# Performance work log

Hardware: AMD Instinct MI355X
Metric: run time of the kernel (lower is better)

## Reference

```python
import jax, jax.numpy as jnp
import numpy as np

N_NODES = 100000
N_EDGES = 1600000
D_IN, D_HID, D_OUT = 256, 256, 128


def setup_inputs() -> dict:
    key = jax.random.key(0)
    k1, k2, k3, k4, k5, k6 = jax.random.split(key, 6)
    x = jax.random.normal(k1, (N_NODES, D_IN), dtype=jnp.float32)
    edge_index = jax.random.randint(k2, (2, N_EDGES), 0, N_NODES, dtype=jnp.int64)
    W1 = jax.random.normal(k3, (D_IN, D_HID), dtype=jnp.float32) / np.sqrt(D_IN)
    b1 = jax.random.normal(k4, (D_HID,), dtype=jnp.float32) * 0.01
    W2 = jax.random.normal(k5, (D_HID, D_OUT), dtype=jnp.float32) / np.sqrt(D_HID)
    b2 = jax.random.normal(k6, (D_OUT,), dtype=jnp.float32) * 0.01
    return {"x": x, "edge_index": edge_index, "W1": W1, "b1": b1, "W2": W2, "b2": b2}


def _gcn_conv(x, src, dst, W, b, n_nodes):
    # PyG GCNConv: linear transform, add self-loops, symmetric normalization,
    # scatter-add aggregation, bias.
    h = x @ W                                         # [N, D_out]
    # degree including self-loop (edge weight 1)
    deg = jax.ops.segment_sum(jnp.ones((src.shape[0],), h.dtype), dst,
                              num_segments=n_nodes) + 1.0
    dinv = jax.lax.rsqrt(deg)                         # [N]
    norm = dinv[src] * dinv[dst]                      # [E]
    msg = h[src] * norm[:, None]                      # [E, D_out] gather + scale
    agg = jax.ops.segment_sum(msg, dst, num_segments=n_nodes)
    # self-loop contribution: norm_ii = dinv_i^2
    agg = agg + h * (dinv * dinv)[:, None]
    return agg + b


def reference(x, edge_index, W1, b1, W2, b2):
    src, dst = edge_index[0], edge_index[1]
    n = x.shape[0]
    h = _gcn_conv(x, src, dst, W1, b1, n)
    h = jax.nn.relu(h)
    out = _gcn_conv(h, src, dst, W2, b2, n)
    return out
```

## Files before the change

kernel.cpp:

```cpp
#include <hip/hip_runtime.h>

#define N_NODES 100000
#define N_EDGES 1600000
#define D_IN 256
#define D_HID 256
#define D_OUT 128
#define SLOTS 64

#define NB 1024
#define NPB 98
#define CAP 2048
#define BIN_T 8192
#define BIN_BLKS ((N_EDGES + BIN_T - 1) / BIN_T)
#define GEMM1_ROWTILES ((N_NODES + 127) / 128)
#define GEMM1_BLKS (GEMM1_ROWTILES * 2)

typedef unsigned int u32;
typedef unsigned short u16;
typedef __attribute__((ext_vector_type(8))) short bf16x8;
typedef __attribute__((ext_vector_type(8))) unsigned short u16x8;
typedef __attribute__((ext_vector_type(4))) float f32x4;

__device__ __forceinline__ u16 f2bf(float v) {
    u32 u = __float_as_uint(v);
    u32 r = (u + 0x7fffu + ((u >> 16) & 1u)) >> 16;
    return (u16)r;
}
__device__ __forceinline__ float bf2f(u16 b) {
    return __uint_as_float(((u32)b) << 16);
}

__global__ __launch_bounds__(256) void weights_kernel(
    const float* __restrict__ W1, u16* __restrict__ w1hi,
    const float* __restrict__ W2, u16* __restrict__ w2hi,
    int* __restrict__ gcnt) {
    const int gtid = blockIdx.x * 256 + threadIdx.x;
    const int gstride = gridDim.x * 256;
    for (int i = gtid; i < NB; i += gstride) gcnt[i] = 0;
    for (int i = gtid; i < D_IN * D_HID; i += gstride) {
        const int k = i / D_HID, n = i - k * D_HID;
        w1hi[(size_t)n * D_IN + k] = f2bf(W1[i]);
    }
    for (int i = gtid; i < D_HID * D_OUT; i += gstride) {
        const int k = i / D_OUT, n = i - k * D_OUT;
        w2hi[(size_t)n * D_HID + k] = f2bf(W2[i]);
    }
}

__global__ __launch_bounds__(256) void fused_bin_gemm1(
    const int* __restrict__ src, const int* __restrict__ dst,
    int* __restrict__ gcnt, int* __restrict__ binned,
    const float* __restrict__ x, const u16* __restrict__ B,
    u16* __restrict__ Cb) {
    __shared__ char smem[49152];
    const int t = threadIdx.x;

    if (blockIdx.x < BIN_BLKS) {
        int* hist = (int*)smem;
        int* cur = hist + NB;
        const int base = blockIdx.x * BIN_T;
#pragma unroll
        for (int q = 0; q < NB / 256; ++q) hist[q * 256 + t] = 0;
        __syncthreads();
#pragma unroll 4
        for (int j = 0; j < BIN_T / 256; ++j) {
            const int e = base + j * 256 + t;
            if (e < N_EDGES) atomicAdd(&hist[dst[e] / NPB], 1);
        }
        __syncthreads();
#pragma unroll
        for (int q = 0; q < NB / 256; ++q) {
            const int b = q * 256 + t;
            const int c = hist[b];
            cur[b] = c ? atomicAdd(&gcnt[b], c) : 0;
        }
        __syncthreads();
#pragma unroll 4
        for (int j = 0; j < BIN_T / 256; ++j) {
            const int e = base + j * 256 + t;
            if (e < N_EDGES) {
                const int d = dst[e];
                const int b = d / NPB;
                const int ld = d - b * NPB;
                const int r = atomicAdd(&cur[b], 1);
                if (r < CAP) binned[(size_t)b * CAP + r] = (ld << 17) | src[e];
            }
        }
        return;
    }

    const int bid = blockIdx.x - BIN_BLKS;
    const int mBase = (bid >> 1) * 128;
    const int nBase = (bid & 1) * 128;
    constexpr int ABYTES = 16384;
    constexpr int BUF = ABYTES + 8192;
    const int wave = t >> 6;
    const int lane = t & 63;
    const int wm = wave >> 1, wn = wave & 1;
    const int K = D_IN, N = D_HID, M = N_NODES;

    f32x4 acc[4][4];
#pragma unroll
    for (int i = 0; i < 4; ++i)
#pragma unroll
        for (int j = 0; j < 4; ++j) acc[i][j] = (f32x4){0.f, 0.f, 0.f, 0.f};

    const int lr = lane >> 3;
    const int lp = lane & 7;
    const int lc = lp ^ lr;
    const int lr4 = lane >> 2;
    const int lc4 = (lane & 3) ^ (lr4 & 3);

    auto STAGE = [&](int buf, int kt) {
        const int k0 = kt * 32;
        char* ldsbuf = smem + buf * BUF;
        {
            const int coff = k0 + lc * 4;
#pragma unroll
            for (int q = 0; q < 4; ++q) {
                const int row = wave * 32 + q * 8 + lr;
                int mg = mBase + row;
                if (mg > M - 1) mg = M - 1;
                const float* s = x + (size_t)mg * K + coff;
                char* d = ldsbuf + (wave * 32 + q * 8) * 128;
                __builtin_amdgcn_global_load_lds(
                    (const __attribute__((address_space(1))) u32*)s,
                    (__attribute__((address_space(3))) u32*)d, 16, 0, 0);
            }
        }
        {
            const int coff = k0 + lc4 * 8;
#pragma unroll
            for (int q = 0; q < 2; ++q) {
                const int row = wave * 32 + q * 16 + lr4;
                const int ng = nBase + row;
                const u16* s = B + (size_t)ng * K + coff;
                char* d = ldsbuf + ABYTES + (wave * 32 + q * 16) * 64;
                __builtin_amdgcn_global_load_lds(
                    (const __attribute__((address_space(1))) u32*)s,
                    (__attribute__((address_space(3))) u32*)d, 16, 0, 0);
            }
        }
    };

    auto COMPUTE = [&](int buf) {
        const char* pa = smem + buf * BUF;
        const char* pb = pa + ABYTES;
        const int lm = lane & 15;
        const int c4 = lane >> 4;
        bf16x8 ah[4], bh[4];
#pragma unroll
        for (int i = 0; i < 4; ++i) {
            const int r = wm * 64 + i * 16 + lm;
            const int s = r & 7;
            const f32x4 a0 = *(const f32x4*)(pa + r * 128 + ((2 * c4) ^ s) * 16);
            const f32x4 a1 = *(const f32x4*)(pa + r * 128 + ((2 * c4 + 1) ^ s) * 16);
            bf16x8 h;
#pragma unroll
            for (int j = 0; j < 4; ++j)
                h[j] = (short)((__float_as_uint(a0[j]) + 0x8000u) >> 16);
#pragma unroll
            for (int j = 0; j < 4; ++j)
                h[4 + j] = (short)((__float_as_uint(a1[j]) + 0x8000u) >> 16);
            ah[i] = h;
        }
#pragma unroll
        for (int j = 0; j < 4; ++j) {
            const int r = wn * 64 + j * 16 + lm;
            bh[j] = *(const bf16x8*)(pb + r * 64 + (c4 ^ (r & 3)) * 16);
        }
#pragma unroll
        for (int i = 0; i < 4; ++i)
#pragma unroll
            for (int j = 0; j < 4; ++j)
                acc[i][j] = __builtin_amdgcn_mfma_f32_16x16x32_bf16(ah[i], bh[j], acc[i][j], 0, 0, 0);
    };

    const int NT = K / 32;
    STAGE(0, 0);
#pragma unroll 1
    for (int kt = 0; kt < NT; ++kt) {
        __syncthreads();
        if (kt + 1 < NT) STAGE((kt + 1) & 1, kt + 1);
        COMPUTE(kt & 1);
        __syncthreads();
    }

    const int lm = lane & 15;
    const int c4 = lane >> 4;
#pragma unroll
    for (int i = 0; i < 4; ++i) {
#pragma unroll
        for (int r = 0; r < 4; ++r) {
            const int row = mBase + wm * 64 + i * 16 + c4 * 4 + r;
            if (row < M) {
#pragma unroll
                for (int j = 0; j < 4; ++j) {
                    const int col = nBase + wn * 64 + j * 16 + lm;
                    Cb[(size_t)row * N + col] = f2bf(acc[i][j][r]);
                }
            }
        }
    }
}

__global__ __launch_bounds__(256) void bucket_scatter(const int* __restrict__ gcnt,
                                                      const int* __restrict__ binned,
                                                      int* __restrict__ deg,
                                                      int* __restrict__ slot,
                                                      float* __restrict__ dinv) {
    __shared__ int degw[NPB];
    __shared__ int slotw[NPB * SLOTS];
    const int b = blockIdx.x;
    const int t = threadIdx.x;
    const int nbase = b * NPB;
    for (int i = t; i < NPB; i += 256) degw[i] = 0;
    __syncthreads();
    int cnt = gcnt[b];
    if (cnt > CAP) cnt = CAP;
    const int* ep = &binned[(size_t)b * CAP];
    for (int i = t; i < cnt; i += 256) {
        const int v = ep[i];
        const int ld = v >> 17;
        const int s = v & 0x1FFFF;
        const int pos = atomicAdd(&degw[ld], 1);
        if (pos < SLOTS) slotw[ld * SLOTS + pos] = s;
    }
    __syncthreads();
    const int lim = min(NPB, N_NODES - nbase);
    if (lim <= 0) return;
    for (int i = t; i < lim * SLOTS; i += 256)
        slot[(size_t)nbase * SLOTS + i] = slotw[i];
    for (int i = t; i < lim; i += 256) {
        const int dgv = degw[i];
        deg[nbase + i] = dgv;
        dinv[nbase + i] = rsqrtf((float)dgv + 1.0f);
    }
}

__global__ __launch_bounds__(256) void gemm_bf16(
    const u16* __restrict__ A, const u16* __restrict__ B,
    u16* __restrict__ Cb, int M, int N, int K) {
    constexpr int ABYTES = 8192;
    __shared__ char lds[2][ABYTES + 8192];
    const int t = threadIdx.x;
    const int wave = t >> 6;
    const int lane = t & 63;
    const int wm = wave >> 1, wn = wave & 1;
    const int mBase = blockIdx.y * 128;
    const int nBase = blockIdx.x * 128;

    f32x4 acc[4][4];
#pragma unroll
    for (int i = 0; i < 4; ++i)
#pragma unroll
        for (int j = 0; j < 4; ++j) acc[i][j] = (f32x4){0.f, 0.f, 0.f, 0.f};

    const int lr4 = lane >> 2;
    const int lc4 = (lane & 3) ^ (lr4 & 3);

    auto STAGE = [&](int buf, int kt) {
        const int k0 = kt * 32;
        const int coff = k0 + lc4 * 8;
#pragma unroll
        for (int q = 0; q < 2; ++q) {
            const int row = wave * 32 + q * 16 + lr4;
            int mg = mBase + row;
            if (mg > M - 1) mg = M - 1;
            const u16* s = A + (size_t)mg * K + coff;
            char* d = &lds[buf][(wave * 32 + q * 16) * 64];
            __builtin_amdgcn_global_load_lds(
                (const __attribute__((address_space(1))) u32*)s,
                (__attribute__((address_space(3))) u32*)d, 16, 0, 0);
        }
#pragma unroll
        for (int q = 0; q < 2; ++q) {
            const int row = wave * 32 + q * 16 + lr4;
            const int ng = nBase + row;
            const u16* s = B + (size_t)ng * K + coff;
            char* d = &lds[buf][ABYTES + (wave * 32 + q * 16) * 64];
            __builtin_amdgcn_global_load_lds(
                (const __attribute__((address_space(1))) u32*)s,
                (__attribute__((address_space(3))) u32*)d, 16, 0, 0);
        }
    };

    auto COMPUTE = [&](int buf) {
        const char* pa = &lds[buf][0];
        const char* pb = &lds[buf][ABYTES];
        const int lm = lane & 15;
        const int c4 = lane >> 4;
        bf16x8 ah[4], bh[4];
#pragma unroll
        for (int i = 0; i < 4; ++i) {
            const int r = wm * 64 + i * 16 + lm;
            ah[i] = *(const bf16x8*)(pa + r * 64 + (c4 ^ (r & 3)) * 16);
        }
#pragma unroll
        for (int j = 0; j < 4; ++j) {
            const int r = wn * 64 + j * 16 + lm;
            bh[j] = *(const bf16x8*)(pb + r * 64 + (c4 ^ (r & 3)) * 16);
        }
#pragma unroll
        for (int i = 0; i < 4; ++i)
#pragma unroll
            for (int j = 0; j < 4; ++j)
                acc[i][j] = __builtin_amdgcn_mfma_f32_16x16x32_bf16(ah[i], bh[j], acc[i][j], 0, 0, 0);
    };

    const int NT = K / 32;
    STAGE(0, 0);
#pragma unroll 1
    for (int kt = 0; kt < NT; ++kt) {
        __syncthreads();
        if (kt + 1 < NT) STAGE((kt + 1) & 1, kt + 1);
        COMPUTE(kt & 1);
        __syncthreads();
    }

    const int lm = lane & 15;
    const int c4 = lane >> 4;
#pragma unroll
    for (int i = 0; i < 4; ++i) {
#pragma unroll
        for (int r = 0; r < 4; ++r) {
            const int row = mBase + wm * 64 + i * 16 + c4 * 4 + r;
            if (row < M) {
#pragma unroll
                for (int j = 0; j < 4; ++j) {
                    const int col = nBase + wn * 64 + j * 16 + lm;
                    Cb[(size_t)row * N + col] = f2bf(acc[i][j][r]);
                }
            }
        }
    }
}

__global__ __launch_bounds__(256) void gather_agg_bf16(const u16* __restrict__ h,
                                                       const int* __restrict__ deg,
                                                       const int* __restrict__ slot,
                                                       const float* __restrict__ dinv,
                                                       const float* __restrict__ bias,
                                                       u16* __restrict__ ob, int n) {
    const int node = blockIdx.x * 8 + (threadIdx.x >> 5);
    const int lane = threadIdx.x & 31;
    if (node >= n) return;
    const float di = dinv[node];
    int dg = deg[node];
    if (dg > SLOTS) dg = SLOTS;
    const int* sp = &slot[(size_t)node * SLOTS];
    const int off = lane * 8;

    float acc[8];
#pragma unroll
    for (int j = 0; j < 8; ++j) acc[j] = 0.f;

    int k = 0;
    for (; k + 1 < dg; k += 2) {
        const int s0 = sp[k];
        const int s1 = sp[k + 1];
        const float n0 = dinv[s0] * di;
        const float n1 = dinv[s1] * di;
        const u16x8 va = *(const u16x8*)&h[(size_t)s0 * 256 + off];
        const u16x8 vb = *(const u16x8*)&h[(size_t)s1 * 256 + off];
#pragma unroll
        for (int j = 0; j < 8; ++j)
            acc[j] += bf2f(va[j]) * n0 + bf2f(vb[j]) * n1;
    }
    if (k < dg) {
        const int s0 = sp[k];
        const float n0 = dinv[s0] * di;
        const u16x8 va = *(const u16x8*)&h[(size_t)s0 * 256 + off];
#pragma unroll
        for (int j = 0; j < 8; ++j) acc[j] += bf2f(va[j]) * n0;
    }

    const float sl = di * di;
    const u16x8 hv = *(const u16x8*)&h[(size_t)node * 256 + off];
    const float4 bv0 = *(const float4*)&bias[off];
    const float4 bv1 = *(const float4*)&bias[off + 4];
    const float bb[8] = {bv0.x, bv0.y, bv0.z, bv0.w, bv1.x, bv1.y, bv1.z, bv1.w};
    u16x8 H;
#pragma unroll
    for (int j = 0; j < 8; ++j)
        H[j] = f2bf(fmaxf(acc[j] + bf2f(hv[j]) * sl + bb[j], 0.f));
    *(u16x8*)&ob[(size_t)node * 256 + off] = H;
}

__global__ __launch_bounds__(256) void gather_agg_out(const u16* __restrict__ h,
                                                      const int* __restrict__ deg,
                                                      const int* __restrict__ slot,
                                                      const float* __restrict__ dinv,
                                                      const float* __restrict__ bias,
                                                      float* __restrict__ outp, int n) {
    const int node = blockIdx.x * 16 + (threadIdx.x >> 4);
    const int lane = threadIdx.x & 15;
    if (node >= n) return;
    const float di = dinv[node];
    int dg = deg[node];
    if (dg > SLOTS) dg = SLOTS;
    const int* sp = &slot[(size_t)node * SLOTS];
    const int off = lane * 8;

    float acc[8];
#pragma unroll
    for (int j = 0; j < 8; ++j) acc[j] = 0.f;

    int k = 0;
    for (; k + 1 < dg; k += 2) {
        const int s0 = sp[k];
        const int s1 = sp[k + 1];
        const float n0 = dinv[s0] * di;
        const float n1 = dinv[s1] * di;
        const u16x8 va = *(const u16x8*)&h[(size_t)s0 * 128 + off];
        const u16x8 vb = *(const u16x8*)&h[(size_t)s1 * 128 + off];
#pragma unroll
        for (int j = 0; j < 8; ++j)
            acc[j] += bf2f(va[j]) * n0 + bf2f(vb[j]) * n1;
    }
    if (k < dg) {
        const int s0 = sp[k];
        const float n0 = dinv[s0] * di;
        const u16x8 va = *(const u16x8*)&h[(size_t)s0 * 128 + off];
#pragma unroll
        for (int j = 0; j < 8; ++j) acc[j] += bf2f(va[j]) * n0;
    }

    const float sl = di * di;
    const u16x8 hv = *(const u16x8*)&h[(size_t)node * 128 + off];
    const float4 bv0 = *(const float4*)&bias[off];
    const float4 bv1 = *(const float4*)&bias[off + 4];
    const float bb[8] = {bv0.x, bv0.y, bv0.z, bv0.w, bv1.x, bv1.y, bv1.z, bv1.w};
    float o[8];
#pragma unroll
    for (int j = 0; j < 8; ++j) o[j] = acc[j] + bf2f(hv[j]) * sl + bb[j];
    float4 o0 = make_float4(o[0], o[1], o[2], o[3]);
    float4 o1 = make_float4(o[4], o[5], o[6], o[7]);
    *(float4*)&outp[(size_t)node * 128 + off] = o0;
    *(float4*)&outp[(size_t)node * 128 + off + 4] = o1;
}

extern "C" void kernel_launch(void* const* d_in, const int* in_sizes, int n_in,
                              void* d_out, int out_size, void* d_ws, size_t ws_size,
                              hipStream_t stream) {
    const float* x  = (const float*)d_in[0];
    const int*   ei = (const int*)d_in[1];
    const float* W1 = (const float*)d_in[2];
    const float* b1 = (const float*)d_in[3];
    const float* W2 = (const float*)d_in[4];
    const float* b2 = (const float*)d_in[5];
    float* out = (float*)d_out;

    const int* src = ei;
    const int* dst = ei + N_EDGES;

    char* ws = (char*)d_ws;
    float* dinv = (float*)(ws + 0x000000);
    int*   deg  = (int*)  (ws + 0x080000);
    int*   gcnt = (int*)  (ws + 0x100000);
    u16* wt1hi = (u16*)(ws + 0x200000);
    u16* wt2hi = (u16*)(ws + 0x240000);
    int* binned = (int*)(ws + 0x280000);
    int* slot   = (int*)(ws + 0xB00000);
    const size_t big = 0x2500000;
    u16* Phi = (u16*)(ws + big);
    u16* Hb  = (u16*)(ws + big + 51200000);

    weights_kernel<<<96, 256, 0, stream>>>(W1, wt1hi, W2, wt2hi, gcnt);

    fused_bin_gemm1<<<BIN_BLKS + GEMM1_BLKS, 256, 0, stream>>>(
        src, dst, gcnt, binned, x, wt1hi, Hb);

    bucket_scatter<<<NB, 256, 0, stream>>>(gcnt, binned, deg, slot, dinv);

    gather_agg_bf16<<<(N_NODES + 7) / 8, 256, 0, stream>>>(
        Hb, deg, slot, dinv, b1, Phi, N_NODES);

    {
        dim3 g(D_OUT / 128, (N_NODES + 127) / 128);
        gemm_bf16<<<g, 256, 0, stream>>>(Phi, wt2hi, Hb, N_NODES, D_OUT, D_HID);
    }
    gather_agg_out<<<(N_NODES + 15) / 16, 256, 0, stream>>>(
        Hb, deg, slot, dinv, b2, out, N_NODES);
}
```

Before: 303.5 us.

## Widen GEMM1 tiles to full N and split them across bin and bucket kernels

GEMM1 tiles now cover all 256 output columns (128x256 per block), so each fp32 x row tile is loaded and converted to bf16 once instead of twice. The row tiles are split into two sets: the first 272 run alongside the edge-binning kernel, and the rest are fused into the bucket-scatter kernel so they overlap its latency-bound work. This balances load across the two launches and removes the duplicate A-tile traffic, at the cost of 64KB of LDS per block and a 4x8 accumulator array per wave, which raise register pressure and may lower occupancy.

```diff
diff --git a/kernel.cpp b/kernel.cpp
--- a/kernel.cpp
+++ b/kernel.cpp
@@ -12,8 +12,9 @@
 #define CAP 2048
 #define BIN_T 8192
 #define BIN_BLKS ((N_EDGES + BIN_T - 1) / BIN_T)
-#define GEMM1_ROWTILES ((N_NODES + 127) / 128)
-#define GEMM1_BLKS (GEMM1_ROWTILES * 2)
+#define G1_TILES ((N_NODES + 127) / 128)
+#define G1_A 272
+#define G1_B (G1_TILES - G1_A)
 
 typedef unsigned int u32;
 typedef unsigned short u16;
@@ -47,12 +48,127 @@
     }
 }
 
+__device__ __forceinline__ void gemm1_tile(int rowTile, const float* __restrict__ x,
+                                           const u16* __restrict__ B,
+                                           u16* __restrict__ Cb, char* smem, int t) {
+    constexpr int ABYTES = 16384;
+    constexpr int BUF = ABYTES + 16384;
+    const int wave = t >> 6;
+    const int lane = t & 63;
+    const int wm = wave >> 1, wn = wave & 1;
+    const int mBase = rowTile * 128;
+    const int K = D_IN, N = D_HID, M = N_NODES;
+
+    f32x4 acc[4][8];
+#pragma unroll
+    for (int i = 0; i < 4; ++i)
+#pragma unroll
+        for (int j = 0; j < 8; ++j) acc[i][j] = (f32x4){0.f, 0.f, 0.f, 0.f};
+
+    const int lr = lane >> 3;
+    const int lp = lane & 7;
+    const int lc = lp ^ lr;
+    const int lr4 = lane >> 2;
+    const int lc4 = (lane & 3) ^ (lr4 & 3);
+
+    auto STAGE = [&](int buf, int kt) {
+        const int k0 = kt * 32;
+        char* lb = smem + buf * BUF;
+        {
+            const int coff = k0 + lc * 4;
+#pragma unroll
+            for (int q = 0; q < 4; ++q) {
+                const int row = wave * 32 + q * 8 + lr;
+                int mg = mBase + row;
+                if (mg > M - 1) mg = M - 1;
+                const float* s = x + (size_t)mg * K + coff;
+                char* d = lb + row * 128;
+                __builtin_amdgcn_global_load_lds(
+                    (const __attribute__((address_space(1))) u32*)s,
+                    (__attribute__((address_space(3))) u32*)d, 16, 0, 0);
+            }
+        }
+        {
+            const int coff = k0 + lc4 * 8;
+#pragma unroll
+            for (int q = 0; q < 4; ++q) {
+                const int row = wave * 64 + q * 16 + lr4;
+                const u16* s = B + (size_t)row * K + coff;
+                char* d = lb + ABYTES + row * 64;
+                __builtin_amdgcn_global_load_lds(
+                    (const __attribute__((address_space(1))) u32*)s,
+                    (__attribute__((address_space(3))) u32*)d, 16, 0, 0);
+            }
+        }
+    };
+
+    auto COMPUTE = [&](int buf) {
+        const char* pa = smem + buf * BUF;
+        const char* pb = pa + ABYTES;
+        const int lm = lane & 15;
+        const int c4 = lane >> 4;
+        bf16x8 ah[4], bh[8];
+#pragma unroll
+        for (int i = 0; i < 4; ++i) {
+            const int r = wm * 64 + i * 16 + lm;
+            const int s = r & 7;
+            const f32x4 a0 = *(const f32x4*)(pa + r * 128 + ((2 * c4) ^ s) * 16);
+            const f32x4 a1 = *(const f32x4*)(pa + r * 128 + ((2 * c4 + 1) ^ s) * 16);
+            bf16x8 h;
+#pragma unroll
+            for (int j = 0; j < 4; ++j)
+                h[j] = (short)((__float_as_uint(a0[j]) + 0x8000u) >> 16);
+#pragma unroll
+            for (int j = 0; j < 4; ++j)
+                h[4 + j] = (short)((__float_as_uint(a1[j]) + 0x8000u) >> 16);
+            ah[i] = h;
+        }
+#pragma unroll
+        for (int j = 0; j < 8; ++j) {
+            const int c = wn * 128 + j * 16 + lm;
+            bh[j] = *(const bf16x8*)(pb + c * 64 + (c4 ^ (c & 3)) * 16);
+        }
+#pragma unroll
+        for (int i = 0; i < 4; ++i)
+#pragma unroll
+            for (int j = 0; j < 8; ++j)
+                acc[i][j] = __builtin_amdgcn_mfma_f32_16x16x32_bf16(ah[i], bh[j], acc[i][j], 0, 0, 0);
+    };
+
+    const int NT = K / 32;
+    STAGE(0, 0);
+#pragma unroll 1
+    for (int kt = 0; kt < NT; ++kt) {
+        __syncthreads();
+        if (kt + 1 < NT) STAGE((kt + 1) & 1, kt + 1);
+        COMPUTE(kt & 1);
+        __syncthreads();
+    }
+
+    const int lm = lane & 15;
+    const int c4 = lane >> 4;
+#pragma unroll
+    for (int i = 0; i < 4; ++i) {
+#pragma unroll
+        for (int r = 0; r < 4; ++r) {
+            const int row = mBase + wm * 64 + i * 16 + c4 * 4 + r;
+            if (row < M) {
+#pragma unroll
+                for (int j = 0; j < 8; ++j) {
+                    const int col = wn * 128 + j * 16 + lm;
+                    Cb[(size_t)row * N + col] = f2bf(acc[i][j][r]);
+                }
+            }
+        }
+    }
+}
+
 __global__ __launch_bounds__(256) void fused_bin_gemm1(
     const int* __restrict__ src, const int* __restrict__ dst,
     int* __restrict__ gcnt, int* __restrict__ binned,
     const float* __restrict__ x, const u16* __restrict__ B,
     u16* __restrict__ Cb) {
-    __shared__ char smem[49152];
+    __shared__ char smem[65536];
     const int t = threadIdx.x;
 
     if (blockIdx.x < BIN_BLKS) {
@@ -88,154 +204,47 @@
         }
         return;
     }
-
-    const int bid = blockIdx.x - BIN_BLKS;
-    const int mBase = (bid >> 1) * 128;
-    const int nBase = (bid & 1) * 128;
-    constexpr int ABYTES = 16384;
-    constexpr int BUF = ABYTES + 8192;
-    const int wave = t >> 6;
-    const int lane = t & 63;
-    const int wm = wave >> 1, wn = wave & 1;
-    const int K = D_IN, N = D_HID, M = N_NODES;
-
-    f32x4 acc[4][4];
-#pragma unroll
-    for (int i = 0; i < 4; ++i)
-#pragma unroll
-        for (int j = 0; j < 4; ++j) acc[i][j] = (f32x4){0.f, 0.f, 0.f, 0.f};
-
-    const int lr = lane >> 3;
-    const int lp = lane & 7;
-    const int lc = lp ^ lr;
-    const int lr4 = lane >> 2;
-    const int lc4 = (lane & 3) ^ (lr4 & 3);
-
-    auto STAGE = [&](int buf, int kt) {
-        const int k0 = kt * 32;
-        char* ldsbuf = smem + buf * BUF;
-        {
-            const int coff = k0 + lc * 4;
-#pragma unroll
-            for (int q = 0; q < 4; ++q) {
-                const int row = wave * 32 + q * 8 + lr;
-                int mg = mBase + row;
-                if (mg > M - 1) mg = M - 1;
-                const float* s = x + (size_t)mg * K + coff;
-                char* d = ldsbuf + (wave * 32 + q * 8) * 128;
-                __builtin_amdgcn_global_load_lds(
-                    (const __attribute__((address_space(1))) u32*)s,
-                    (__attribute__((address_space(3))) u32*)d, 16, 0, 0);
-            }
-        }
-        {
-            const int coff = k0 + lc4 * 8;
-#pragma unroll
-            for (int q = 0; q < 2; ++q) {
-                const int row = wave * 32 + q * 16 + lr4;
-                const int ng = nBase + row;
-                const u16* s = B + (size_t)ng * K + coff;
-                char* d = ldsbuf + ABYTES + (wave * 32 + q * 16) * 64;
-                __builtin_amdgcn_global_load_lds(
-                    (const __attribute__((address_space(1))) u32*)s,
-                    (__attribute__((address_space(3))) u32*)d, 16, 0, 0);
-            }
-        }
-    };
-
-    auto COMPUTE = [&](int buf) {
-        const char* pa = smem + buf * BUF;
-        const char* pb = pa + ABYTES;
-        const int lm = lane & 15;
-        const int c4 = lane >> 4;
-        bf16x8 ah[4], bh[4];
-#pragma unroll
-        for (int i = 0; i < 4; ++i) {
-            const int r = wm * 64 + i * 16 + lm;
-            const int s = r & 7;
-            const f32x4 a0 = *(const f32x4*)(pa + r * 128 + ((2 * c4) ^ s) * 16);
-            const f32x4 a1 = *(const f32x4*)(pa + r * 128 + ((2 * c4 + 1) ^ s) * 16);
-            bf16x8 h;
-#pragma unroll
-            for (int j = 0; j < 4; ++j)
-                h[j] = (short)((__float_as_uint(a0[j]) + 0x8000u) >> 16);
-#pragma unroll
-            for (int j = 0; j < 4; ++j)
-                h[4 + j] = (short)((__float_as_uint(a1[j]) + 0x8000u) >> 16);
-            ah[i] = h;
-        }
-#pragma unroll
-        for (int j = 0; j < 4; ++j) {
-            const int r = wn * 64 + j * 16 + lm;
-            bh[j] = *(const bf16x8*)(pb + r * 64 + (c4 ^ (r & 3)) * 16);
-        }
-#pragma unroll
-        for (int i = 0; i < 4; ++i)
-#pragma unroll
-            for (int j = 0; j < 4; ++j)
-                acc[i][j] = __builtin_amdgcn_mfma_f32_16x16x32_bf16(ah[i], bh[j], acc[i][j], 0, 0, 0);
-    };
-
-    const int NT = K / 32;
-    STAGE(0, 0);
-#pragma unroll 1
-    for (int kt = 0; kt < NT; ++kt) {
-        __syncthreads();
-        if (kt + 1 < NT) STAGE((kt + 1) & 1, kt + 1);
-        COMPUTE(kt & 1);
-        __syncthreads();
-    }
-
-    const int lm = lane & 15;
-    const int c4 = lane >> 4;
-#pragma unroll
-    for (int i = 0; i < 4; ++i) {
-#pragma unroll
-        for (int r = 0; r < 4; ++r) {
-            const int row = mBase + wm * 64 + i * 16 + c4 * 4 + r;
-            if (row < M) {
-#pragma unroll
-                for (int j = 0; j < 4; ++j) {
-                    const int col = nBase + wn * 64 + j * 16 + lm;
-                    Cb[(size_t)row * N + col] = f2bf(acc[i][j][r]);
-                }
-            }
-        }
-    }
-}
-
-__global__ __launch_bounds__(256) void bucket_scatter(const int* __restrict__ gcnt,
-                                                      const int* __restrict__ binned,
-                                                      int* __restrict__ deg,
-                                                      int* __restrict__ slot,
-                                                      float* __restrict__ dinv) {
-    __shared__ int degw[NPB];
-    __shared__ int slotw[NPB * SLOTS];
-    const int b = blockIdx.x;
+    gemm1_tile(blockIdx.x - BIN_BLKS, x, B, Cb, smem, t);
+}
+
+__global__ __launch_bounds__(256) void fused_bucket_gemm1(
+    const int* __restrict__ gcnt, const int* __restrict__ binned,
+    int* __restrict__ deg, int* __restrict__ slot, float* __restrict__ dinv,
+    const float* __restrict__ x, const u16* __restrict__ B,
+    u16* __restrict__ Cb) {
+    __shared__ char smem[65536];
     const int t = threadIdx.x;
-    const int nbase = b * NPB;
-    for (int i = t; i < NPB; i += 256) degw[i] = 0;
-    __syncthreads();
-    int cnt = gcnt[b];
-    if (cnt > CAP) cnt = CAP;
-    const int* ep = &binned[(size_t)b * CAP];
-    for (int i = t; i < cnt; i += 256) {
-        const int v = ep[i];
-        const int ld = v >> 17;
-        const int s = v & 0x1FFFF;
-        const int pos = atomicAdd(&degw[ld], 1);
-        if (pos < SLOTS) slotw[ld * SLOTS + pos] = s;
-    }
-    __syncthreads();
-    const int lim = min(NPB, N_NODES - nbase);
-    if (lim <= 0) return;
-    for (int i = t; i < lim * SLOTS; i += 256)
-        slot[(size_t)nbase * SLOTS + i] = slotw[i];
-    for (int i = t; i < lim; i += 256) {
-        const int dgv = degw[i];
-        deg[nbase + i] = dgv;
-        dinv[nbase + i] = rsqrtf((float)dgv + 1.0f);
-    }
+
+    if (blockIdx.x < NB) {
+        int* degw = (int*)smem;
+        int* slotw = degw + 128;
+        const int b = blockIdx.x;
+        const int nbase = b * NPB;
+        for (int i = t; i < NPB; i += 256) degw[i] = 0;
+        __syncthreads();
+        int cnt = gcnt[b];
+        if (cnt > CAP) cnt = CAP;
+        const int* ep = &binned[(size_t)b * CAP];
+        for (int i = t; i < cnt; i += 256) {
+            const int v = ep[i];
+            const int ld = v >> 17;
+            const int s = v & 0x1FFFF;
+            const int pos = atomicAdd(&degw[ld], 1);
+            if (pos < SLOTS) slotw[ld * SLOTS + pos] = s;
+        }
+        __syncthreads();
+        const int lim = min(NPB, N_NODES - nbase);
+        if (lim <= 0) return;
+        for (int i = t; i < lim * SLOTS; i += 256)
+            slot[(size_t)nbase * SLOTS + i] = slotw[i];
+        for (int i = t; i < lim; i += 256) {
+            const int dgv = degw[i];
+            deg[nbase + i] = dgv;
+            dinv[nbase + i] = rsqrtf((float)dgv + 1.0f);
+        }
+        return;
+    }
+    gemm1_tile(G1_A + (blockIdx.x - NB), x, B, Cb, smem, t);
 }
 
 __global__ __launch_bounds__(256) void gemm_bf16(
@@ -468,10 +477,11 @@
 
     weights_kernel<<<96, 256, 0, stream>>>(W1, wt1hi, W2, wt2hi, gcnt);
 
-    fused_bin_gemm1<<<BIN_BLKS + GEMM1_BLKS, 256, 0, stream>>>(
+    fused_bin_gemm1<<<BIN_BLKS + G1_A, 256, 0, stream>>>(
         src, dst, gcnt, binned, x, wt1hi, Hb);
 
-    bucket_scatter<<<NB, 256, 0, stream>>>(gcnt, binned, deg, slot, dinv);
+    fused_bucket_gemm1<<<NB + G1_B, 256, 0, stream>>>(
+        gcnt, binned, deg, slot, dinv, x, wt1hi, Hb);
 
     gather_agg_bf16<<<(N_NODES + 7) / 8, 256, 0, stream>>>(
         Hb, deg, slot, dinv, b1, Phi, N_NODES);
```

Result: slower. 322.1 us (+6.1%).

## Split GEMM1 tiles across bin and bucket-scatter kernels to balance load

Applied to the files above, without the earlier changes.

Moves the GEMM1 tile body into a shared device function. The first 520 tiles now run alongside edge binning, and the remaining tiles run inside a new fused kernel alongside bucket scatter. The goal is to fill idle compute units during the lightweight bucket-scatter phase and shorten the first fused launch. The split point is a fixed constant, and bucket-scatter blocks now use 48KB of LDS, which may reduce their occupancy.

```diff
diff --git a/kernel.cpp b/kernel.cpp
--- a/kernel.cpp
+++ b/kernel.cpp
@@ -14,6 +14,8 @@
 #define BIN_BLKS ((N_EDGES + BIN_T - 1) / BIN_T)
 #define GEMM1_ROWTILES ((N_NODES + 127) / 128)
 #define GEMM1_BLKS (GEMM1_ROWTILES * 2)
+#define G1_A 520
+#define G1_B (GEMM1_BLKS - G1_A)
 
 typedef unsigned int u32;
 typedef unsigned short u16;
@@ -47,6 +49,123 @@
     }
 }
 
+__device__ __forceinline__ void gemm1_tile(int bid, const float* __restrict__ x,
+                                           const u16* __restrict__ B,
+                                           u16* __restrict__ Cb, char* smem, int t) {
+    const int mBase = (bid >> 1) * 128;
+    const int nBase = (bid & 1) * 128;
+    constexpr int ABYTES = 16384;
+    constexpr int BUF = ABYTES + 8192;
+    const int wave = t >> 6;
+    const int lane = t & 63;
+    const int wm = wave >> 1, wn = wave & 1;
+    const int K = D_IN, N = D_HID, M = N_NODES;
+
+    f32x4 acc[4][4];
+#pragma unroll
+    for (int i = 0; i < 4; ++i)
+#pragma unroll
+        for (int j = 0; j < 4; ++j) acc[i][j] = (f32x4){0.f, 0.f, 0.f, 0.f};
+
+    const int lr = lane >> 3;
+    const int lp = lane & 7;
+    const int lc = lp ^ lr;
+    const int lr4 = lane >> 2;
+    const int lc4 = (lane & 3) ^ (lr4 & 3);
+
+    auto STAGE = [&](int buf, int kt) {
+        const int k0 = kt * 32;
+        char* ldsbuf = smem + buf * BUF;
+        {
+            const int coff = k0 + lc * 4;
+#pragma unroll
+            for (int q = 0; q < 4; ++q) {
+                const int row = wave * 32 + q * 8 + lr;
+                int mg = mBase + row;
+                if (mg > M - 1) mg = M - 1;
+                const float* s = x + (size_t)mg * K + coff;
+                char* d = ldsbuf + (wave * 32 + q * 8) * 128;
+                __builtin_amdgcn_global_load_lds(
+                    (const __attribute__((address_space(1))) u32*)s,
+                    (__attribute__((address_space(3))) u32*)d, 16, 0, 0);
+            }
+        }
+        {
+            const int coff = k0 + lc4 * 8;
+#pragma unroll
+            for (int q = 0; q < 2; ++q) {
+                const int row = wave * 32 + q * 16 + lr4;
+                const int ng = nBase + row;
+                const u16* s = B + (size_t)ng * K + coff;
+                char* d = ldsbuf + ABYTES + (wave * 32 + q * 16) * 64;
+                __builtin_amdgcn_global_load_lds(
+                    (const __attribute__((address_space(1))) u32*)s,
+                    (__attribute__((address_space(3))) u32*)d, 16, 0, 0);
+            }
+        }
+    };
+
+    auto COMPUTE = [&](int buf) {
+        const char* pa = smem + buf * BUF;
+        const char* pb = pa + ABYTES;
+        const int lm = lane & 15;
+        const int c4 = lane >> 4;
+        bf16x8 ah[4], bh[4];
+#pragma unroll
+        for (int i = 0; i < 4; ++i) {
+            const int r = wm * 64 + i * 16 + lm;
+            const int s = r & 7;
+            const f32x4 a0 = *(const f32x4*)(pa + r * 128 + ((2 * c4) ^ s) * 16);
+            const f32x4 a1 = *(const f32x4*)(pa + r * 128 + ((2 * c4 + 1) ^ s) * 16);
+            bf16x8 h;
+#pragma unroll
+            for (int j = 0; j < 4; ++j)
+                h[j] = (short)((__float_as_uint(a0[j]) + 0x8000u) >> 16);
+#pragma unroll
+            for (int j = 0; j < 4; ++j)
+                h[4 + j] = (short)((__float_as_uint(a1[j]) + 0x8000u) >> 16);
+            ah[i] = h;
+        }
+#pragma unroll
+        for (int j = 0; j < 4; ++j) {
+            const int r = wn * 64 + j * 16 + lm;
+            bh[j] = *(const bf16x8*)(pb + r * 64 + (c4 ^ (r & 3)) * 16);
+        }
+#pragma unroll
+        for (int i = 0; i < 4; ++i)
+#pragma unroll
+            for (int j = 0; j < 4; ++j)
+                acc[i][j] = __builtin_amdgcn_mfma_f32_16x16x32_bf16(ah[i], bh[j], acc[i][j], 0, 0, 0);
+    };
+
+    const int NT = K / 32;
+    STAGE(0, 0);
+#pragma unroll 1
+    for (int kt = 0; kt < NT; ++kt) {
+        __syncthreads();
+        if (kt + 1 < NT) STAGE((kt + 1) & 1, kt + 1);
+        COMPUTE(kt & 1);
+        __syncthreads();
+    }
+
+    const int lm = lane & 15;
+    const int c4 = lane >> 4;
+#pragma unroll
+    for (int i = 0; i < 4; ++i) {
+#pragma unroll
+        for (int r = 0; r < 4; ++r) {
+            const int row = mBase + wm * 64 + i * 16 + c4 * 4 + r;
+            if (row < M) {
+#pragma unroll
+                for (int j = 0; j < 4; ++j) {
+                    const int col = nBase + wn * 64 + j * 16 + lm;
+                    Cb[(size_t)row * N + col] = f2bf(acc[i][j][r]);
+                }
+            }
+        }
+    }
+}
+
 __global__ __launch_bounds__(256) void fused_bin_gemm1(
     const int* __restrict__ src, const int* __restrict__ dst,
     int* __restrict__ gcnt, int* __restrict__ binned,
@@ -88,154 +207,47 @@
         }
         return;
     }
-
-    const int bid = blockIdx.x - BIN_BLKS;
-    const int mBase = (bid >> 1) * 128;
-    const int nBase = (bid & 1) * 128;
-    constexpr int ABYTES = 16384;
-    constexpr int BUF = ABYTES + 8192;
-    const int wave = t >> 6;
-    const int lane = t & 63;
-    const int wm = wave >> 1, wn = wave & 1;
-    const int K = D_IN, N = D_HID, M = N_NODES;
-
-    f32x4 acc[4][4];
-#pragma unroll
-    for (int i = 0; i < 4; ++i)
-#pragma unroll
-        for (int j = 0; j < 4; ++j) acc[i][j] = (f32x4){0.f, 0.f, 0.f, 0.f};
-
-    const int lr = lane >> 3;
-    const int lp = lane & 7;
-    const int lc = lp ^ lr;
-    const int lr4 = lane >> 2;
-    const int lc4 = (lane & 3) ^ (lr4 & 3);
-
-    auto STAGE = [&](int buf, int kt) {
-        const int k0 = kt * 32;
-        char* ldsbuf = smem + buf * BUF;
-        {
-            const int coff = k0 + lc * 4;
-#pragma unroll
-            for (int q = 0; q < 4; ++q) {
-                const int row = wave * 32 + q * 8 + lr;
-                int mg = mBase + row;
-                if (mg > M - 1) mg = M - 1;
-                const float* s = x + (size_t)mg * K + coff;
-                char* d = ldsbuf + (wave * 32 + q * 8) * 128;
-                __builtin_amdgcn_global_load_lds(
-                    (const __attribute__((address_space(1))) u32*)s,
-                    (__attribute__((address_space(3))) u32*)d, 16, 0, 0);
-            }
-        }
-        {
-            const int coff = k0 + lc4 * 8;
-#pragma unroll
-            for (int q = 0; q < 2; ++q) {
-                const int row = wave * 32 + q * 16 + lr4;
-                const int ng = nBase + row;
-                const u16* s = B + (size_t)ng * K + coff;
-                char* d = ldsbuf + ABYTES + (wave * 32 + q * 16) * 64;
-                __builtin_amdgcn_global_load_lds(
-                    (const __attribute__((address_space(1))) u32*)s,
-                    (__attribute__((address_space(3))) u32*)d, 16, 0, 0);
-            }
-        }
-    };
-
-    auto COMPUTE = [&](int buf) {
-        const char* pa = smem + buf * BUF;
-        const char* pb = pa + ABYTES;
-        const int lm = lane & 15;
-        const int c4 = lane >> 4;
-        bf16x8 ah[4], bh[4];
-#pragma unroll
-        for (int i = 0; i < 4; ++i) {
-            const int r = wm * 64 + i * 16 + lm;
-            const int s = r & 7;
-            const f32x4 a0 = *(const f32x4*)(pa + r * 128 + ((2 * c4) ^ s) * 16);
-            const f32x4 a1 = *(const f32x4*)(pa + r * 128 + ((2 * c4 + 1) ^ s) * 16);
-            bf16x8 h;
-#pragma unroll
-            for (int j = 0; j < 4; ++j)
-                h[j] = (short)((__float_as_uint(a0[j]) + 0x8000u) >> 16);
-#pragma unroll
-            for (int j = 0; j < 4; ++j)
-                h[4 + j] = (short)((__float_as_uint(a1[j]) + 0x8000u) >> 16);
-            ah[i] = h;
-        }
-#pragma unroll
-        for (int j = 0; j < 4; ++j) {
-            const int r = wn * 64 + j * 16 + lm;
-            bh[j] = *(const bf16x8*)(pb + r * 64 + (c4 ^ (r & 3)) * 16);
-        }
-#pragma unroll
-        for (int i = 0; i < 4; ++i)
-#pragma unroll
-            for (int j = 0; j < 4; ++j)
-                acc[i][j] = __builtin_amdgcn_mfma_f32_16x16x32_bf16(ah[i], bh[j], acc[i][j], 0, 0, 0);
-    };
-
-    const int NT = K / 32;
-    STAGE(0, 0);
-#pragma unroll 1
-    for (int kt = 0; kt < NT; ++kt) {
-        __syncthreads();
-        if (kt + 1 < NT) STAGE((kt + 1) & 1, kt + 1);
-        COMPUTE(kt & 1);
-        __syncthreads();
-    }
-
-    const int lm = lane & 15;
-    const int c4 = lane >> 4;
-#pragma unroll
-    for (int i = 0; i < 4; ++i) {
-#pragma unroll
-        for (int r = 0; r < 4; ++r) {
-            const int row = mBase + wm * 64 + i * 16 + c4 * 4 + r;
-            if (row < M) {
-#pragma unroll
-                for (int j = 0; j < 4; ++j) {
-                    const int col = nBase + wn * 64 + j * 16 + lm;
-                    Cb[(size_t)row * N + col] = f2bf(acc[i][j][r]);
-                }
-            }
-        }
-    }
-}
-
-__global__ __launch_bounds__(256) void bucket_scatter(const int* __restrict__ gcnt,
-                                                      const int* __restrict__ binned,
-                                                      int* __restrict__ deg,
-                                                      int* __restrict__ slot,
-                                                      float* __restrict__ dinv) {
-    __shared__ int degw[NPB];
-    __shared__ int slotw[NPB * SLOTS];
-    const int b = blockIdx.x;
+    gemm1_tile(blockIdx.x - BIN_BLKS, x, B, Cb, smem, t);
+}
+
+__global__ __launch_bounds__(256) void fused_bucket_gemm1(
+    const int* __restrict__ gcnt, const int* __restrict__ binned,
+    int* __restrict__ deg, int* __restrict__ slot, float* __restrict__ dinv,
+    const float* __restrict__ x, const u16* __restrict__ B,
+    u16* __restrict__ Cb) {
+    __shared__ char smem[49152];
     const int t = threadIdx.x;
-    const int nbase = b * NPB;
-    for (int i = t; i < NPB; i += 256) degw[i] = 0;
-    __syncthreads();
-    int cnt = gcnt[b];
-    if (cnt > CAP) cnt = CAP;
-    const int* ep = &binned[(size_t)b * CAP];
-    for (int i = t; i < cnt; i += 256) {
-        const int v = ep[i];
-        const int ld = v >> 17;
-        const int s = v & 0x1FFFF;
-        const int pos = atomicAdd(&degw[ld], 1);
-        if (pos < SLOTS) slotw[ld * SLOTS + pos] = s;
-    }
-    __syncthreads();
-    const int lim = min(NPB, N_NODES - nbase);
-    if (lim <= 0) return;
-    for (int i = t; i < lim * SLOTS; i += 256)
-        slot[(size_t)nbase * SLOTS + i] = slotw[i];
-    for (int i = t; i < lim; i += 256) {
-        const int dgv = degw[i];
-        deg[nbase + i] = dgv;
-        dinv[nbase + i] = rsqrtf((float)dgv + 1.0f);
-    }
+
+    if (blockIdx.x < NB) {
+        int* degw = (int*)smem;
+        int* slotw = degw + 128;
+        const int b = blockIdx.x;
+        const int nbase = b * NPB;
+        for (int i = t; i < NPB; i += 256) degw[i] = 0;
+        __syncthreads();
+        int cnt = gcnt[b];
+        if (cnt > CAP) cnt = CAP;
+        const int* ep = &binned[(size_t)b * CAP];
+        for (int i = t; i < cnt; i += 256) {
+            const int v = ep[i];
+            const int ld = v >> 17;
+            const int s = v & 0x1FFFF;
+            const int pos = atomicAdd(&degw[ld], 1);
+            if (pos < SLOTS) slotw[ld * SLOTS + pos] = s;
+        }
+        __syncthreads();
+        const int lim = min(NPB, N_NODES - nbase);
+        if (lim <= 0) return;
+        for (int i = t; i < lim * SLOTS; i += 256)
+            slot[(size_t)nbase * SLOTS + i] = slotw[i];
+        for (int i = t; i < lim; i += 256) {
+            const int dgv = degw[i];
+            deg[nbase + i] = dgv;
+            dinv[nbase + i] = rsqrtf((float)dgv + 1.0f);
+        }
+        return;
+    }
+    gemm1_tile(G1_A + (blockIdx.x - NB), x, B, Cb, smem, t);
 }
 
 __global__ __launch_bounds__(256) void gemm_bf16(
@@ -468,10 +480,11 @@
 
     weights_kernel<<<96, 256, 0, stream>>>(W1, wt1hi, W2, wt2hi, gcnt);
 
-    fused_bin_gemm1<<<BIN_BLKS + GEMM1_BLKS, 256, 0, stream>>>(
+    fused_bin_gemm1<<<BIN_BLKS + G1_A, 256, 0, stream>>>(
         src, dst, gcnt, binned, x, wt1hi, Hb);
 
-    bucket_scatter<<<NB, 256, 0, stream>>>(gcnt, binned, deg, slot, dinv);
+    fused_bucket_gemm1<<<NB + G1_B, 256, 0, stream>>>(
+        gcnt, binned, deg, slot, dinv, x, wt1hi, Hb);
 
     gather_agg_bf16<<<(N_NODES + 7) / 8, 256, 0, stream>>>(
         Hb, deg, slot, dinv, b1, Phi, N_NODES);
```

After: 315.1 us. 1.04x slower.
